# Kernel tuning notes

Measured on AMD Instinct MI355X. Metric: run time of the kernel, lower is better.

Reference implementation:

```python
import jax, jax.numpy as jnp
import numpy as np

N_NODES = 100000
N_EDGES = 1600000
NODE_IN = 64
EDGE_DIM = 32
NODE_OUT = 64


def setup_inputs() -> dict:
    key = jax.random.key(0)
    ks = jax.random.split(key, 8)
    return {
        "nfeats": jax.random.normal(ks[0], (N_NODES, NODE_IN), dtype=jnp.float32),
        "efeats": jax.random.normal(ks[1], (N_EDGES, EDGE_DIM), dtype=jnp.float32),
        "src": jax.random.randint(ks[2], (N_EDGES,), 0, N_NODES, dtype=jnp.int32),
        "dst": jax.random.randint(ks[3], (N_EDGES,), 0, N_NODES, dtype=jnp.int32),
        "W_msg_w": jax.random.normal(ks[4], (NODE_IN + EDGE_DIM, NODE_OUT), dtype=jnp.float32) * 0.1,
        "W_msg_b": jax.random.normal(ks[5], (NODE_OUT,), dtype=jnp.float32) * 0.1,
        "W_apply_w": jax.random.normal(ks[6], (NODE_IN + NODE_OUT, NODE_OUT), dtype=jnp.float32) * 0.1,
        "W_apply_b": jax.random.normal(ks[7], (NODE_OUT,), dtype=jnp.float32) * 0.1,
    }


def reference(nfeats, efeats, src, dst, W_msg_w, W_msg_b, W_apply_w, W_apply_b):
    n_nodes = nfeats.shape[0]
    # message: gather source node features, concat edge features, linear
    m = jnp.concatenate([nfeats[src], efeats], axis=-1) @ W_msg_w + W_msg_b  # [E, node_out]
    # per-destination mean (DGL fn.mean); zero for isolated nodes
    s = jax.ops.segment_sum(m, dst, num_segments=n_nodes)                     # [N, node_out]
    cnt = jax.ops.segment_sum(jnp.ones((m.shape[0],), m.dtype), dst, num_segments=n_nodes)
    h_neigh = s / jnp.maximum(cnt, 1.0)[:, None]
    # apply: concat self features with aggregated messages, linear, activation
    h = jnp.concatenate([nfeats, h_neigh], axis=-1) @ W_apply_w + W_apply_b   # [N, node_out]
    return jax.nn.relu(h)
```

## Files before the change

kernel.cpp:

```cpp
#include <hip/hip_runtime.h>

#define NN 100000
#define NE 1600000
#define NBIN 782
#define CAP  3072
#define EPB  8192
#define NBLKE 196

#define OFF_RS      0
#define OFF_BINSZ   100004
#define OFF_BINBASE 100788
#define OFF_MASK    101572
#define OFF_EINFO   300520
#define OFF_G       3500520
#define OFF_HM      OFF_G
#define OFF_OM      (OFF_G + 153272)
#define OFF_WCOMB   13100520
#define OFF_BMW     13110760

__global__ __launch_bounds__(256) void k_bhist(const int4* __restrict__ dst4,
                                               int* __restrict__ hm) {
  __shared__ int h[NBIN];
  int b = blockIdx.x, t = threadIdx.x;
  for (int i = t; i < NBIN; i += 256) h[i] = 0;
  __syncthreads();
  int e0 = b * EPB;
#pragma unroll
  for (int i = 0; i < EPB / 1024; ++i) {
    int f = i * 256 + t;
    int e = e0 + f * 4;
    if (e < NE) {
      int4 d = dst4[(e0 >> 2) + f];
      atomicAdd(&h[d.x >> 7], 1);
      atomicAdd(&h[d.y >> 7], 1);
      atomicAdd(&h[d.z >> 7], 1);
      atomicAdd(&h[d.w >> 7], 1);
    }
  }
  __syncthreads();
  for (int i = t; i < NBIN; i += 256) hm[b * NBIN + i] = h[i];
}

__global__ __launch_bounds__(256) void k_bscan(const int* __restrict__ hm,
                                               int* __restrict__ om,
                                               int* __restrict__ binsz) {
  int w = (blockIdx.x * 256 + threadIdx.x) >> 6;
  int lane = threadIdx.x & 63;
  if (w >= NBIN) return;
  int carry = 0;
  for (int base = 0; base < NBLKE; base += 64) {
    int b = base + lane;
    int v = (b < NBLKE) ? hm[b * NBIN + w] : 0;
    int inc = v;
#pragma unroll
    for (int off = 1; off < 64; off <<= 1) {
      int x = __shfl_up(inc, off);
      if (lane >= off) inc += x;
    }
    if (b < NBLKE) om[b * NBIN + w] = carry + inc - v;
    carry += __shfl(inc, 63);
  }
  if (lane == 0) binsz[w] = carry;
}

__global__ __launch_bounds__(1024) void k_binscan(const int* __restrict__ binsz,
                                                  int* __restrict__ binbase) {
  __shared__ int s[1024];
  int t = threadIdx.x;
  int v = (t < NBIN) ? binsz[t] : 0;
  s[t] = v; __syncthreads();
#pragma unroll
  for (int off = 1; off < 1024; off <<= 1) {
    int x = (t >= off) ? s[t - off] : 0;
    __syncthreads();
    s[t] += x;
    __syncthreads();
  }
  if (t <= NBIN) binbase[t] = s[t] - v;
}

__global__ __launch_bounds__(256) void k_bplace(
    const int4* __restrict__ src4, const int4* __restrict__ dst4,
    const int* __restrict__ om, const int* __restrict__ binbase,
    int2* __restrict__ einfo) {
  __shared__ int2 buf[EPB];
  __shared__ int hstart[1024];
  __shared__ int hcur[1024];
  __shared__ int obase[NBIN];
  __shared__ int tscan[256];
  int b = blockIdx.x, t = threadIdx.x;
  int e0 = b * EPB;
  for (int i = t; i < 1024; i += 256) hcur[i] = 0;
  for (int i = t; i < NBIN; i += 256) obase[i] = binbase[i] + om[b * NBIN + i];
  __syncthreads();
#pragma unroll
  for (int i = 0; i < EPB / 1024; ++i) {
    int f = i * 256 + t;
    int e = e0 + f * 4;
    if (e < NE) {
      int4 d = dst4[(e0 >> 2) + f];
      atomicAdd(&hcur[d.x >> 7], 1);
      atomicAdd(&hcur[d.y >> 7], 1);
      atomicAdd(&hcur[d.z >> 7], 1);
      atomicAdd(&hcur[d.w >> 7], 1);
    }
  }
  __syncthreads();
  int base4 = t * 4;
  int v0 = hcur[base4], v1 = hcur[base4 + 1], v2 = hcur[base4 + 2], v3 = hcur[base4 + 3];
  int s = v0 + v1 + v2 + v3;
  tscan[t] = s;
  __syncthreads();
#pragma unroll
  for (int off = 1; off < 256; off <<= 1) {
    int x = (t >= off) ? tscan[t - off] : 0;
    __syncthreads();
    tscan[t] += x;
    __syncthreads();
  }
  int texcl = tscan[t] - s;
  hstart[base4]     = texcl;
  hstart[base4 + 1] = texcl + v0;
  hstart[base4 + 2] = texcl + v0 + v1;
  hstart[base4 + 3] = texcl + v0 + v1 + v2;
  __syncthreads();
  for (int i = t; i < 1024; i += 256) hcur[i] = hstart[i];
  __syncthreads();
#pragma unroll
  for (int i = 0; i < EPB / 1024; ++i) {
    int f = i * 256 + t;
    int e = e0 + f * 4;
    if (e < NE) {
      int4 d = dst4[(e0 >> 2) + f];
      int4 sv = src4[(e0 >> 2) + f];
      int p0 = atomicAdd(&hcur[d.x >> 7], 1);
      int p1 = atomicAdd(&hcur[d.y >> 7], 1);
      int p2 = atomicAdd(&hcur[d.z >> 7], 1);
      int p3 = atomicAdd(&hcur[d.w >> 7], 1);
      buf[p0] = make_int2(sv.x | ((d.x & 127) << 20), (e)     | ((d.x >> 7) << 21));
      buf[p1] = make_int2(sv.y | ((d.y & 127) << 20), (e + 1) | ((d.y >> 7) << 21));
      buf[p2] = make_int2(sv.z | ((d.z & 127) << 20), (e + 2) | ((d.z >> 7) << 21));
      buf[p3] = make_int2(sv.w | ((d.w & 127) << 20), (e + 3) | ((d.w >> 7) << 21));
    }
  }
  __syncthreads();
  int nE = NE - e0; if (nE > EPB) nE = EPB;
  for (int i = t; i < nE; i += 256) {
    int2 r = buf[i];
    int bin = (unsigned)r.y >> 21;
    int pos = obase[bin] + (i - hstart[bin]);
    einfo[pos] = make_int2(r.x, r.y & 0x1FFFFF);
  }
}

__global__ __launch_bounds__(256) void k_sortbin(const int* __restrict__ binbase,
                                                 int* __restrict__ rs,
                                                 float* __restrict__ mask,
                                                 int2* __restrict__ einfo) {
  __shared__ int hist[128];
  __shared__ int excl[128];
  __shared__ int2 buf[CAP];
  int b = blockIdx.x, t = threadIdx.x;
  int base = binbase[b];
  int nE = binbase[b + 1] - base;
  int nS = nE < CAP ? nE : CAP;
  if (t < 128) hist[t] = 0;
  __syncthreads();
  for (int i = t; i < nS; i += 256) {
    int2 v = einfo[base + i];
    buf[i] = v;
    atomicAdd(&hist[(v.x >> 20) & 127], 1);
  }
  __syncthreads();
  int myc = 0;
  if (t < 128) { myc = hist[t]; excl[t] = myc; }
  __syncthreads();
#pragma unroll
  for (int off = 1; off < 128; off <<= 1) {
    int x = 0;
    if (t < 128 && t >= off) x = excl[t - off];
    __syncthreads();
    if (t < 128) excl[t] += x;
    __syncthreads();
  }
  if (t < 128) {
    int node = b * 128 + t;
    if (node < NN) {
      rs[node] = base + excl[t] - myc;
      mask[node] = myc ? 1.f : 0.f;
    }
    hist[t] = t ? excl[t - 1] : 0;
  }
  if (b == NBIN - 1 && t == 0) rs[NN] = NE;
  __syncthreads();
  for (int i = t; i < nS; i += 256) {
    int2 v = buf[i];
    int dl = (v.x >> 20) & 127;
    int p = atomicAdd(&hist[dl], 1);
    einfo[base + p] = make_int2(v.x & 0xFFFFF, v.y);
  }
  for (int i = nS + t; i < nE; i += 256)
    atomicAnd((int*)&einfo[base + i].x, 0xFFFFF);
}

__global__ __launch_bounds__(256) void k_gather(
    const float* __restrict__ nf, const float* __restrict__ ef,
    const int2* __restrict__ einfo, const int* __restrict__ rs,
    float* __restrict__ g) {
  int wid = threadIdx.x >> 6, lane = threadIdx.x & 63;
  int node = blockIdx.x * 4 + wid;
  int beg = rs[node], end = rs[node + 1];
  int deg = end - beg;
  bool hi = lane >= 32;
  int l32 = lane & 31;
  float a0 = 0.f, a1 = 0.f;
  for (int base = 0; base < deg; base += 64) {
    int nb = deg - base; if (nb > 64) nb = 64;
    int2 info = (lane < nb) ? einfo[beg + base + lane] : make_int2(0, 0);
    int j = 0;
    for (; j + 16 <= nb; j += 16) {
      int s0  = __builtin_amdgcn_readlane(info.x, j);
      int s1  = __builtin_amdgcn_readlane(info.x, j + 1);
      int s2  = __builtin_amdgcn_readlane(info.x, j + 2);
      int s3  = __builtin_amdgcn_readlane(info.x, j + 3);
      int s4  = __builtin_amdgcn_readlane(info.x, j + 4);
      int s5  = __builtin_amdgcn_readlane(info.x, j + 5);
      int s6  = __builtin_amdgcn_readlane(info.x, j + 6);
      int s7  = __builtin_amdgcn_readlane(info.x, j + 7);
      int s8  = __builtin_amdgcn_readlane(info.x, j + 8);
      int s9  = __builtin_amdgcn_readlane(info.x, j + 9);
      int s10 = __builtin_amdgcn_readlane(info.x, j + 10);
      int s11 = __builtin_amdgcn_readlane(info.x, j + 11);
      int s12 = __builtin_amdgcn_readlane(info.x, j + 12);
      int s13 = __builtin_amdgcn_readlane(info.x, j + 13);
      int s14 = __builtin_amdgcn_readlane(info.x, j + 14);
      int s15 = __builtin_amdgcn_readlane(info.x, j + 15);
      int ep0 = hi ? __builtin_amdgcn_readlane(info.y, j + 1)
                   : __builtin_amdgcn_readlane(info.y, j);
      int ep1 = hi ? __builtin_amdgcn_readlane(info.y, j + 3)
                   : __builtin_amdgcn_readlane(info.y, j + 2);
      int ep2 = hi ? __builtin_amdgcn_readlane(info.y, j + 5)
                   : __builtin_amdgcn_readlane(info.y, j + 4);
      int ep3 = hi ? __builtin_amdgcn_readlane(info.y, j + 7)
                   : __builtin_amdgcn_readlane(info.y, j + 6);
      int ep4 = hi ? __builtin_amdgcn_readlane(info.y, j + 9)
                   : __builtin_amdgcn_readlane(info.y, j + 8);
      int ep5 = hi ? __builtin_amdgcn_readlane(info.y, j + 11)
                   : __builtin_amdgcn_readlane(info.y, j + 10);
      int ep6 = hi ? __builtin_amdgcn_readlane(info.y, j + 13)
                   : __builtin_amdgcn_readlane(info.y, j + 12);
      int ep7 = hi ? __builtin_amdgcn_readlane(info.y, j + 15)
                   : __builtin_amdgcn_readlane(info.y, j + 14);
      float v0  = nf[s0  * 64 + lane];
      float v1  = nf[s1  * 64 + lane];
      float v2  = nf[s2  * 64 + lane];
      float v3  = nf[s3  * 64 + lane];
      float v4  = nf[s4  * 64 + lane];
      float v5  = nf[s5  * 64 + lane];
      float v6  = nf[s6  * 64 + lane];
      float v7  = nf[s7  * 64 + lane];
      float v8  = nf[s8  * 64 + lane];
      float v9  = nf[s9  * 64 + lane];
      float v10 = nf[s10 * 64 + lane];
      float v11 = nf[s11 * 64 + lane];
      float v12 = nf[s12 * 64 + lane];
      float v13 = nf[s13 * 64 + lane];
      float v14 = nf[s14 * 64 + lane];
      float v15 = nf[s15 * 64 + lane];
      float w0 = ef[ep0 * 32 + l32];
      float w1 = ef[ep1 * 32 + l32];
      float w2 = ef[ep2 * 32 + l32];
      float w3 = ef[ep3 * 32 + l32];
      float w4 = ef[ep4 * 32 + l32];
      float w5 = ef[ep5 * 32 + l32];
      float w6 = ef[ep6 * 32 + l32];
      float w7 = ef[ep7 * 32 + l32];
      a0 += ((v0 + v1) + (v2 + v3)) + ((v4 + v5) + (v6 + v7))
          + ((v8 + v9) + (v10 + v11)) + ((v12 + v13) + (v14 + v15));
      a1 += ((w0 + w1) + (w2 + w3)) + ((w4 + w5) + (w6 + w7));
    }
    for (; j + 4 <= nb; j += 4) {
      int s0 = __builtin_amdgcn_readlane(info.x, j);
      int s1 = __builtin_amdgcn_readlane(info.x, j + 1);
      int s2 = __builtin_amdgcn_readlane(info.x, j + 2);
      int s3 = __builtin_amdgcn_readlane(info.x, j + 3);
      int ep0 = hi ? __builtin_amdgcn_readlane(info.y, j + 1)
                   : __builtin_amdgcn_readlane(info.y, j);
      int ep1 = hi ? __builtin_amdgcn_readlane(info.y, j + 3)
                   : __builtin_amdgcn_readlane(info.y, j + 2);
      float v0 = nf[s0 * 64 + lane];
      float v1 = nf[s1 * 64 + lane];
      float v2 = nf[s2 * 64 + lane];
      float v3 = nf[s3 * 64 + lane];
      float w0 = ef[ep0 * 32 + l32];
      float w1 = ef[ep1 * 32 + l32];
      a0 += (v0 + v1) + (v2 + v3);
      a1 += w0 + w1;
    }
    for (; j < nb; ++j) {
      int s0 = __builtin_amdgcn_readlane(info.x, j);
      int e0 = __builtin_amdgcn_readlane(info.y, j);
      a0 += nf[s0 * 64 + lane];
      if (!hi) a1 += ef[e0 * 32 + l32];
    }
  }
  a1 += __shfl_down(a1, 32);
  float inv = deg > 0 ? 1.f / (float)deg : 0.f;
  g[node * 96 + lane] = a0 * inv;
  if (!hi) g[node * 96 + 64 + l32] = a1 * inv;
}

__global__ __launch_bounds__(256) void k_pre1(
    const float* __restrict__ Wm, const float* __restrict__ bm,
    const float* __restrict__ Wa, float* __restrict__ Wcomb,
    float* __restrict__ bmW) {
  int b = blockIdx.x, t = threadIdx.x;
  if (b < 24) {
    int o = b * 256 + t;
    int k = o >> 6, j = o & 63;
    float acc = 0.f;
    for (int kk = 0; kk < 64; ++kk)
      acc += Wm[k * 64 + kk] * Wa[(64 + kk) * 64 + j];
    Wcomb[(64 + k) * 64 + j] = acc;
  } else {
    for (int i = t; i < 64 * 64; i += 256) Wcomb[i] = Wa[i];
    if (t < 64) {
      float acc = 0.f;
      for (int kk = 0; kk < 64; ++kk) acc += bm[kk] * Wa[(64 + kk) * 64 + t];
      bmW[t] = acc;
    }
  }
}

__global__ __launch_bounds__(256) void k_main(
    const float4* __restrict__ nf4, const float4* __restrict__ g4,
    const float* __restrict__ mask,
    const float4* __restrict__ Wcomb4, const float* __restrict__ bmW,
    const float* __restrict__ ba, float* __restrict__ out) {
  __shared__ float sA[128 * 33];
  __shared__ float sB[32 * 64];
  int tid = threadIdx.x;
  int ty = tid >> 3, tx = tid & 7;
  int nbase = blockIdx.x * 128;
  float acc[4][8];
#pragma unroll
  for (int r = 0; r < 4; ++r)
#pragma unroll
    for (int e = 0; e < 8; ++e) acc[r][e] = 0.f;

  for (int c = 0; c < 5; ++c) {
#pragma unroll
    for (int i = 0; i < 4; ++i) {
      int f = i * 256 + tid;
      int nl = f >> 3, q = f & 7;
      int node = nbase + nl; if (node > NN - 1) node = NN - 1;
      float4 v;
      if (c < 2) {
        v = nf4[node * 16 + c * 8 + q];
      } else {
        v = g4[node * 24 + (c - 2) * 8 + q];
      }
      float* p = &sA[nl * 33 + q * 4];
      p[0] = v.x; p[1] = v.y; p[2] = v.z; p[3] = v.w;
    }
#pragma unroll
    for (int i = 0; i < 2; ++i) {
      int f = i * 256 + tid;
      int kk = f >> 4, j4 = f & 15;
      float4 w = Wcomb4[(c * 32 + kk) * 16 + j4];
      *(float4*)&sB[kk * 64 + j4 * 4] = w;
    }
    __syncthreads();
#pragma unroll 8
    for (int kk = 0; kk < 32; ++kk) {
      float4 b0 = *(const float4*)&sB[kk * 64 + tx * 8];
      float4 b1 = *(const float4*)&sB[kk * 64 + tx * 8 + 4];
#pragma unroll
      for (int r = 0; r < 4; ++r) {
        float a = sA[(ty * 4 + r) * 33 + kk];
        acc[r][0] += a * b0.x; acc[r][1] += a * b0.y;
        acc[r][2] += a * b0.z; acc[r][3] += a * b0.w;
        acc[r][4] += a * b1.x; acc[r][5] += a * b1.y;
        acc[r][6] += a * b1.z; acc[r][7] += a * b1.w;
      }
    }
    __syncthreads();
  }
  float4 ba0 = ((const float4*)ba)[tx * 2];
  float4 ba1 = ((const float4*)ba)[tx * 2 + 1];
  float4 bw0 = ((const float4*)bmW)[tx * 2];
  float4 bw1 = ((const float4*)bmW)[tx * 2 + 1];
#pragma unroll
  for (int r = 0; r < 4; ++r) {
    int node = nbase + ty * 4 + r;
    if (node < NN) {
      float mk = mask[node];
      float4 o0, o1;
      o0.x = acc[r][0] + ba0.x + mk * bw0.x;
      o0.y = acc[r][1] + ba0.y + mk * bw0.y;
      o0.z = acc[r][2] + ba0.z + mk * bw0.z;
      o0.w = acc[r][3] + ba0.w + mk * bw0.w;
      o1.x = acc[r][4] + ba1.x + mk * bw1.x;
      o1.y = acc[r][5] + ba1.y + mk * bw1.y;
      o1.z = acc[r][6] + ba1.z + mk * bw1.z;
      o1.w = acc[r][7] + ba1.w + mk * bw1.w;
      o0.x = fmaxf(o0.x, 0.f); o0.y = fmaxf(o0.y, 0.f);
      o0.z = fmaxf(o0.z, 0.f); o0.w = fmaxf(o0.w, 0.f);
      o1.x = fmaxf(o1.x, 0.f); o1.y = fmaxf(o1.y, 0.f);
      o1.z = fmaxf(o1.z, 0.f); o1.w = fmaxf(o1.w, 0.f);
      *(float4*)&out[node * 64 + tx * 8] = o0;
      *(float4*)&out[node * 64 + tx * 8 + 4] = o1;
    }
  }
}

extern "C" void kernel_launch(void* const* d_in, const int* in_sizes, int n_in,
                              void* d_out, int out_size, void* d_ws, size_t ws_size,
                              hipStream_t stream) {
  const float* nf = (const float*)d_in[0];
  const float* ef = (const float*)d_in[1];
  const int*   src = (const int*)d_in[2];
  const int*   dst = (const int*)d_in[3];
  const float* Wm = (const float*)d_in[4];
  const float* bm = (const float*)d_in[5];
  const float* Wa = (const float*)d_in[6];
  const float* ba = (const float*)d_in[7];
  int*   wsi = (int*)d_ws;
  float* wsf = (float*)d_ws;
  int*   rs      = wsi + OFF_RS;
  int*   binsz   = wsi + OFF_BINSZ;
  int*   binbase = wsi + OFF_BINBASE;
  int2*  einfo   = (int2*)(wsi + OFF_EINFO);
  int*   hm      = wsi + OFF_HM;
  int*   om      = wsi + OFF_OM;
  float* mask    = wsf + OFF_MASK;
  float* g       = wsf + OFF_G;
  float* Wcomb   = wsf + OFF_WCOMB;
  float* bmW     = wsf + OFF_BMW;
  float* out = (float*)d_out;

  k_pre1<<<25, 256, 0, stream>>>(Wm, bm, Wa, Wcomb, bmW);
  k_bhist<<<NBLKE, 256, 0, stream>>>((const int4*)dst, hm);
  k_bscan<<<(NBIN * 64 + 255) / 256, 256, 0, stream>>>(hm, om, binsz);
  k_binscan<<<1, 1024, 0, stream>>>(binsz, binbase);
  k_bplace<<<NBLKE, 256, 0, stream>>>((const int4*)src, (const int4*)dst, om,
                                      binbase, einfo);
  k_sortbin<<<NBIN, 256, 0, stream>>>(binbase, rs, mask, einfo);
  k_gather<<<NN / 4, 256, 0, stream>>>(nf, ef, einfo, rs, g);
  k_main<<<(NN + 127) / 128, 256, 0, stream>>>(
      (const float4*)nf, (const float4*)g, mask,
      (const float4*)Wcomb, bmW, ba, out);
}
```

Baseline: 178.6 us.

## Process four consecutive nodes per wavefront in gather kernel with shared edge chunks

Each wavefront in the gather kernel now handles four consecutive destination nodes instead of one. It loads their CSR edge range as contiguous 64-edge chunks and flushes a node's mean whenever its boundary is crossed. The goal is to cut the waste of mostly idle edge-info loads and lanes for low-degree nodes (average degree 16) and to reduce the number of waves launched. In exchange there is more control flow per chunk, the unroll depth drops to 8, and there are extra branches and shuffles at node boundaries.

```diff
diff --git a/kernel.cpp b/kernel.cpp
--- a/kernel.cpp
+++ b/kernel.cpp
@@ -208,106 +208,95 @@
     const int2* __restrict__ einfo, const int* __restrict__ rs,
     float* __restrict__ g) {
   int wid = threadIdx.x >> 6, lane = threadIdx.x & 63;
-  int node = blockIdx.x * 4 + wid;
-  int beg = rs[node], end = rs[node + 1];
-  int deg = end - beg;
+  int n0 = (blockIdx.x * 4 + wid) * 4;
+  int r = (lane < 5) ? rs[n0 + lane] : 0;
+  int beg = __builtin_amdgcn_readlane(r, 0);
+  int end = __builtin_amdgcn_readlane(r, 4);
   bool hi = lane >= 32;
   int l32 = lane & 31;
   float a0 = 0.f, a1 = 0.f;
-  for (int base = 0; base < deg; base += 64) {
-    int nb = deg - base; if (nb > 64) nb = 64;
-    int2 info = (lane < nb) ? einfo[beg + base + lane] : make_int2(0, 0);
-    int j = 0;
-    for (; j + 16 <= nb; j += 16) {
-      int s0  = __builtin_amdgcn_readlane(info.x, j);
-      int s1  = __builtin_amdgcn_readlane(info.x, j + 1);
-      int s2  = __builtin_amdgcn_readlane(info.x, j + 2);
-      int s3  = __builtin_amdgcn_readlane(info.x, j + 3);
-      int s4  = __builtin_amdgcn_readlane(info.x, j + 4);
-      int s5  = __builtin_amdgcn_readlane(info.x, j + 5);
-      int s6  = __builtin_amdgcn_readlane(info.x, j + 6);
-      int s7  = __builtin_amdgcn_readlane(info.x, j + 7);
-      int s8  = __builtin_amdgcn_readlane(info.x, j + 8);
-      int s9  = __builtin_amdgcn_readlane(info.x, j + 9);
-      int s10 = __builtin_amdgcn_readlane(info.x, j + 10);
-      int s11 = __builtin_amdgcn_readlane(info.x, j + 11);
-      int s12 = __builtin_amdgcn_readlane(info.x, j + 12);
-      int s13 = __builtin_amdgcn_readlane(info.x, j + 13);
-      int s14 = __builtin_amdgcn_readlane(info.x, j + 14);
-      int s15 = __builtin_amdgcn_readlane(info.x, j + 15);
-      int ep0 = hi ? __builtin_amdgcn_readlane(info.y, j + 1)
-                   : __builtin_amdgcn_readlane(info.y, j);
-      int ep1 = hi ? __builtin_amdgcn_readlane(info.y, j + 3)
-                   : __builtin_amdgcn_readlane(info.y, j + 2);
-      int ep2 = hi ? __builtin_amdgcn_readlane(info.y, j + 5)
-                   : __builtin_amdgcn_readlane(info.y, j + 4);
-      int ep3 = hi ? __builtin_amdgcn_readlane(info.y, j + 7)
-                   : __builtin_amdgcn_readlane(info.y, j + 6);
-      int ep4 = hi ? __builtin_amdgcn_readlane(info.y, j + 9)
-                   : __builtin_amdgcn_readlane(info.y, j + 8);
-      int ep5 = hi ? __builtin_amdgcn_readlane(info.y, j + 11)
-                   : __builtin_amdgcn_readlane(info.y, j + 10);
-      int ep6 = hi ? __builtin_amdgcn_readlane(info.y, j + 13)
-                   : __builtin_amdgcn_readlane(info.y, j + 12);
-      int ep7 = hi ? __builtin_amdgcn_readlane(info.y, j + 15)
-                   : __builtin_amdgcn_readlane(info.y, j + 14);
-      float v0  = nf[s0  * 64 + lane];
-      float v1  = nf[s1  * 64 + lane];
-      float v2  = nf[s2  * 64 + lane];
-      float v3  = nf[s3  * 64 + lane];
-      float v4  = nf[s4  * 64 + lane];
-      float v5  = nf[s5  * 64 + lane];
-      float v6  = nf[s6  * 64 + lane];
-      float v7  = nf[s7  * 64 + lane];
-      float v8  = nf[s8  * 64 + lane];
-      float v9  = nf[s9  * 64 + lane];
-      float v10 = nf[s10 * 64 + lane];
-      float v11 = nf[s11 * 64 + lane];
-      float v12 = nf[s12 * 64 + lane];
-      float v13 = nf[s13 * 64 + lane];
-      float v14 = nf[s14 * 64 + lane];
-      float v15 = nf[s15 * 64 + lane];
-      float w0 = ef[ep0 * 32 + l32];
-      float w1 = ef[ep1 * 32 + l32];
-      float w2 = ef[ep2 * 32 + l32];
-      float w3 = ef[ep3 * 32 + l32];
-      float w4 = ef[ep4 * 32 + l32];
-      float w5 = ef[ep5 * 32 + l32];
-      float w6 = ef[ep6 * 32 + l32];
-      float w7 = ef[ep7 * 32 + l32];
-      a0 += ((v0 + v1) + (v2 + v3)) + ((v4 + v5) + (v6 + v7))
-          + ((v8 + v9) + (v10 + v11)) + ((v12 + v13) + (v14 + v15));
-      a1 += ((w0 + w1) + (w2 + w3)) + ((w4 + w5) + (w6 + w7));
-    }
-    for (; j + 4 <= nb; j += 4) {
-      int s0 = __builtin_amdgcn_readlane(info.x, j);
-      int s1 = __builtin_amdgcn_readlane(info.x, j + 1);
-      int s2 = __builtin_amdgcn_readlane(info.x, j + 2);
-      int s3 = __builtin_amdgcn_readlane(info.x, j + 3);
-      int ep0 = hi ? __builtin_amdgcn_readlane(info.y, j + 1)
-                   : __builtin_amdgcn_readlane(info.y, j);
-      int ep1 = hi ? __builtin_amdgcn_readlane(info.y, j + 3)
-                   : __builtin_amdgcn_readlane(info.y, j + 2);
-      float v0 = nf[s0 * 64 + lane];
-      float v1 = nf[s1 * 64 + lane];
-      float v2 = nf[s2 * 64 + lane];
-      float v3 = nf[s3 * 64 + lane];
-      float w0 = ef[ep0 * 32 + l32];
-      float w1 = ef[ep1 * 32 + l32];
-      a0 += (v0 + v1) + (v2 + v3);
-      a1 += w0 + w1;
-    }
-    for (; j < nb; ++j) {
-      int s0 = __builtin_amdgcn_readlane(info.x, j);
-      int e0 = __builtin_amdgcn_readlane(info.y, j);
-      a0 += nf[s0 * 64 + lane];
-      if (!hi) a1 += ef[e0 * 32 + l32];
-    }
-  }
-  a1 += __shfl_down(a1, 32);
-  float inv = deg > 0 ? 1.f / (float)deg : 0.f;
-  g[node * 96 + lane] = a0 * inv;
-  if (!hi) g[node * 96 + 64 + l32] = a1 * inv;
+  int curk = 0;
+  int cbeg = beg;
+  int nxt = __builtin_amdgcn_readlane(r, 1);
+  for (int base = beg; base < end; base += 64) {
+    int nb = end - base; if (nb > 64) nb = 64;
+    int2 info = (lane < nb) ? einfo[base + lane] : make_int2(0, 0);
+    int off = 0;
+    while (off < nb) {
+      int stop = nxt - base; if (stop > nb) stop = nb;
+      int j = off;
+      for (; j + 8 <= stop; j += 8) {
+        int s0 = __builtin_amdgcn_readlane(info.x, j);
+        int s1 = __builtin_amdgcn_readlane(info.x, j + 1);
+        int s2 = __builtin_amdgcn_readlane(info.x, j + 2);
+        int s3 = __builtin_amdgcn_readlane(info.x, j + 3);
+        int s4 = __builtin_amdgcn_readlane(info.x, j + 4);
+        int s5 = __builtin_amdgcn_readlane(info.x, j + 5);
+        int s6 = __builtin_amdgcn_readlane(info.x, j + 6);
+        int s7 = __builtin_amdgcn_readlane(info.x, j + 7);
+        int ep0 = hi ? __builtin_amdgcn_readlane(info.y, j + 1)
+                     : __builtin_amdgcn_readlane(info.y, j);
+        int ep1 = hi ? __builtin_amdgcn_readlane(info.y, j + 3)
+                     : __builtin_amdgcn_readlane(info.y, j + 2);
+        int ep2 = hi ? __builtin_amdgcn_readlane(info.y, j + 5)
+                     : __builtin_amdgcn_readlane(info.y, j + 4);
+        int ep3 = hi ? __builtin_amdgcn_readlane(info.y, j + 7)
+                     : __builtin_amdgcn_readlane(info.y, j + 6);
+        float v0 = nf[s0 * 64 + lane];
+        float v1 = nf[s1 * 64 + lane];
+        float v2 = nf[s2 * 64 + lane];
+        float v3 = nf[s3 * 64 + lane];
+        float v4 = nf[s4 * 64 + lane];
+        float v5 = nf[s5 * 64 + lane];
+        float v6 = nf[s6 * 64 + lane];
+        float v7 = nf[s7 * 64 + lane];
+        float w0 = ef[ep0 * 32 + l32];
+        float w1 = ef[ep1 * 32 + l32];
+        float w2 = ef[ep2 * 32 + l32];
+        float w3 = ef[ep3 * 32 + l32];
+        a0 += ((v0 + v1) + (v2 + v3)) + ((v4 + v5) + (v6 + v7));
+        a1 += (w0 + w1) + (w2 + w3);
+      }
+      for (; j + 2 <= stop; j += 2) {
+        int s0 = __builtin_amdgcn_readlane(info.x, j);
+        int s1 = __builtin_amdgcn_readlane(info.x, j + 1);
+        int ep = hi ? __builtin_amdgcn_readlane(info.y, j + 1)
+                    : __builtin_amdgcn_readlane(info.y, j);
+        float v0 = nf[s0 * 64 + lane];
+        float v1 = nf[s1 * 64 + lane];
+        float w0 = ef[ep * 32 + l32];
+        a0 += v0 + v1;
+        a1 += w0;
+      }
+      if (j < stop) {
+        int s0 = __builtin_amdgcn_readlane(info.x, j);
+        int e0 = __builtin_amdgcn_readlane(info.y, j);
+        a0 += nf[s0 * 64 + lane];
+        if (!hi) a1 += ef[e0 * 32 + l32];
+      }
+      off = stop;
+      if (nxt - base <= nb) {
+        float a1f = a1 + __shfl_down(a1, 32);
+        int node = n0 + curk;
+        int degk = nxt - cbeg;
+        float inv = degk > 0 ? 1.f / (float)degk : 0.f;
+        g[node * 96 + lane] = a0 * inv;
+        if (!hi) g[node * 96 + 64 + l32] = a1f * inv;
+        a0 = 0.f; a1 = 0.f;
+        ++curk;
+        cbeg = nxt;
+        if (curk < 4) nxt = __builtin_amdgcn_readlane(r, curk + 1);
+        else break;
+      }
+    }
+    if (curk >= 4) break;
+  }
+  while (curk < 4) {
+    int node = n0 + curk;
+    g[node * 96 + lane] = 0.f;
+    if (!hi) g[node * 96 + 64 + l32] = 0.f;
+    ++curk;
+  }
 }
 
 __global__ __launch_bounds__(256) void k_pre1(
@@ -446,7 +435,7 @@
   k_bplace<<<NBLKE, 256, 0, stream>>>((const int4*)src, (const int4*)dst, om,
                                       binbase, einfo);
   k_sortbin<<<NBIN, 256, 0, stream>>>(binbase, rs, mask, einfo);
-  k_gather<<<NN / 4, 256, 0, stream>>>(nf, ef, einfo, rs, g);
+  k_gather<<<NN / 16, 256, 0, stream>>>(nf, ef, einfo, rs, g);
   k_main<<<(NN + 127) / 128, 256, 0, stream>>>(
       (const float4*)nf, (const float4*)g, mask,
       (const float4*)Wcomb, bmW, ba, out);
```

Result: slower. 185.6 us (+3.9%).
